# Kernel optimization log

Measured on AMD Instinct MI355X. Metric: run time of the kernel, lower is better.

Reference implementation:

```python
import jax, jax.numpy as jnp
import numpy as np

T, B, OBS, H, ACT = 256, 1024, 256, 256, 64
SLOPE = 0.1


def setup_inputs() -> dict:
    key = jax.random.key(0)
    ks = jax.random.split(key, 20)
    stdv = 1.0 / np.sqrt(H)
    u = lambda k, shape: jax.random.uniform(k, shape, jnp.float32, -stdv, stdv)
    return {
        "x": jax.random.normal(ks[0], (T, B, OBS), jnp.float32),
        "noise1": jax.random.uniform(ks[1], (T, B, 1), jnp.float32),
        "noise2": jax.random.uniform(ks[2], (T, B, 1), jnp.float32),
        # FCEncoder: two Linear+ReLU layers
        "We1": u(ks[3], (OBS, H)), "be1": u(ks[4], (H,)),
        "We2": u(ks[5], (H, H)), "be2": u(ks[6], (H,)),
        # cell_1 (bottom): U_11 [bottom,4H+1], U_21 [top,4H+1], W_01 [H,4H+1], bias
        "U11_1": u(ks[7], (H, 4 * H + 1)), "U21_1": u(ks[8], (H, 4 * H + 1)),
        "W01_1": u(ks[9], (H, 4 * H + 1)), "b1": u(ks[10], (4 * H + 1,)),
        # cell_2 (top, last layer): no U_21
        "U11_2": u(ks[11], (H, 4 * H + 1)), "W01_2": u(ks[12], (H, 4 * H + 1)),
        "b2": u(ks[13], (4 * H + 1,)),
        "Wh": u(ks[14], (H, H)), "bh": u(ks[15], (H,)),
        "Wp": u(ks[16], (H, ACT)), "bp": u(ks[17], (ACT,)),
    }


def _trigger_train(z_hat, noise):
    # forward: (noise < z_hat).float(); backward: 0.1 * identity (straight-through)
    hard = (noise < z_hat).astype(z_hat.dtype)
    return jax.lax.stop_gradient(hard) + 0.1 * (z_hat - jax.lax.stop_gradient(z_hat))


def _gates(f_s):
    f = jax.nn.sigmoid(f_s[:, 0:H])
    i = jax.nn.sigmoid(f_s[:, H:2 * H])
    o = jax.nn.sigmoid(f_s[:, 2 * H:3 * H])
    g = jnp.tanh(f_s[:, 3 * H:4 * H])
    z_hat = jnp.clip((SLOPE * f_s[:, 4 * H:4 * H + 1] + 1.0) / 2.0, 0.05, 0.95)
    return f, i, o, g, z_hat


def reference(x, noise1, noise2, We1, be1, We2, be2,
              U11_1, U21_1, W01_1, b1, U11_2, W01_2, b2, Wh, bh, Wp, bp):
    # encoder over all timesteps at once (parallel_wrapper equivalent)
    xe = jax.nn.relu(jnp.einsum('tbi,ih->tbh', x, We1) + be1)
    xe = jax.nn.relu(jnp.einsum('tbi,ih->tbh', xe, We2) + be2)

    def step(carry, inp):
        h1, c1, z1, h2, c2 = carry
        xt, n1, n2 = inp
        # ---- cell 1 (not last layer; z_bottom = 1) ----
        fs1 = h1 @ W01_1 + z1 * (h2 @ U21_1) + xt @ U11_1 + b1
        f, i, o, g, zhat1 = _gates(fs1)
        c1n = f * c1 + i * g              # z_bottom == 1 everywhere
        h1n = o * jnp.tanh(c1n)
        z1n = _trigger_train(zhat1, n1)
        # ---- cell 2 (last layer; z_bottom = z1n, s_topdown = 0) ----
        fs2 = h2 @ W01_2 + z1n * (h1n @ U11_2) + b2
        f2, i2, o2, g2, zhat2 = _gates(fs2)
        c2n = (1.0 - z1n) * c2 + z1n * (f2 * c2 + i2 * g2)
        h2n = o2 * jnp.tanh(c2n)
        _ = _trigger_train(zhat2, n2)
        return (h1n, c1n, z1n, h2n, c2n), h2n

    zeros = jnp.zeros((B, H), jnp.float32)
    init = (zeros, zeros, jnp.ones((B, 1), jnp.float32), zeros, zeros)
    _, emb = jax.lax.scan(step, init, (xe, noise1, noise2))  # emb: [T,B,H]

    hid = jax.nn.relu(jnp.einsum('tbh,hk->tbk', emb, Wh) + bh)
    pred = jnp.tanh(jnp.einsum('tbh,ha->tba', hid, Wp) + bp)
    return pred
```

## Files before the change

### kernel.cpp

```cpp
#include <hip/hip_runtime.h>
#include <math.h>

typedef __attribute__((ext_vector_type(8))) _Float16 half8;
typedef __attribute__((ext_vector_type(4))) float    f32x4;
typedef unsigned long long u64;

#define NSTEP 256
#define CH    32
#define NCHUNK (NSTEP/CH)
#define NB    1024
#define HID   256
#define BH    262144
#define LK    40
#define LK1   776
#define LW2   520
#define INV2K 4.8828125e-4f

#define W1H_OFF 0
#define W1L_OFF 49664
#define W2H_OFF 99328
#define WZ_OFF  132608
#define PAN_OFF 135680
#define SEQ_SMEM 135936

__device__ __forceinline__ float sigf(float x){ return 1.f/(1.f+expf(-x)); }
__device__ __forceinline__ void splitf(float v, _Float16& h, _Float16& l){
    h = (_Float16)v; l = (_Float16)((v - (float)h)*2048.f);
}

__global__ __launch_bounds__(256)
void wsplit_k(const float* __restrict__ s0, const float* __restrict__ s1,
              const float* __restrict__ s2, int K, int N, int ldn,
              int kb1, int kb2, int perm,
              _Float16* __restrict__ oh, _Float16* __restrict__ ol)
{
    int idx = blockIdx.x*256 + threadIdx.x;
    if (idx >= N*K) return;
    int n = idx / K, k = idx - n*K;
    int jsrc = perm ? ((n&3)*256 + (n>>2)) : n;
    const float* s = (k < kb1) ? &s0[(size_t)k*ldn]
                   : (k < kb2) ? &s1[(size_t)(k-kb1)*ldn]
                               : &s2[(size_t)(k-kb2)*ldn];
    float v = s[jsrc];
    _Float16 h, l; splitf(v, h, l);
    oh[idx] = h; ol[idx] = l;
}

__global__ void wz_k(const float* __restrict__ W01, const float* __restrict__ U21,
                     const float* __restrict__ U11, float* __restrict__ wz)
{
    int k = blockIdx.x*256 + threadIdx.x;
    if (k >= 768) return;
    wz[k] = (k < 256) ? W01[(size_t)k*1025 + 1024]
          : (k < 512) ? U21[(size_t)(k-256)*1025 + 1024]
                      : U11[(size_t)(k-512)*1025 + 1024];
}

__global__ __launch_bounds__(256)
void init_k(_Float16* h1H, _Float16* h1L, _Float16* h2H, _Float16* h2L,
            float* c1g, float* c2g, unsigned* zcb)
{
    int i = blockIdx.x*256 + threadIdx.x;
    h1H[i] = (_Float16)0.f; h1L[i] = (_Float16)0.f;
    h2H[i] = (_Float16)0.f; h2L[i] = (_Float16)0.f;
    c1g[i] = 0.f; c2g[i] = 0.f;
    if (i < NB) zcb[i] = 1u;
}

template<int AIN, int AOUT, int NCOL>
__global__ __launch_bounds__(256)
void gemm_t(const float* __restrict__ Af,
            const _Float16* __restrict__ Ah_, const _Float16* __restrict__ Al_,
            const _Float16* __restrict__ Bh_, const _Float16* __restrict__ Bl_,
            const float* __restrict__ bias,
            _Float16* __restrict__ Oh, _Float16* __restrict__ Ol,
            float* __restrict__ Of)
{
    constexpr int NT = 8;
    __shared__ __align__(16) char smem[40960];

    const int tid  = threadIdx.x;
    const size_t R0 = (size_t)blockIdx.x*64;
    const int C0   = blockIdx.y*64;
    const int rh   = (tid>>6)&1, ch = tid>>7;
    const int lane = tid&63, lr = lane&15, kq = (lane>>4)<<3;
    const int arow = tid>>2, seg = tid&3;
    const size_t abase = (R0+arow)*256 + seg*8;
    const size_t wbase = (size_t)(C0 + (tid>>2))*256 + seg*8;

    f32x4 am[2][2], ax[2][2];
#pragma unroll
    for (int r=0;r<2;++r)
#pragma unroll
        for (int c=0;c<2;++c){ am[r][c]=(f32x4)0.f; ax[r][c]=(f32x4)0.f; }

    half8 rah, ral, rwh, rwl;
    auto load_tile = [&](int k0, half8& ah, half8& al, half8& wh, half8& wl) {
        if (AIN == 0) {
            float4 a0 = *(const float4*)(Af + abase + k0);
            float4 a1 = *(const float4*)(Af + abase + k0 + 4);
            float av[8] = {a0.x,a0.y,a0.z,a0.w,a1.x,a1.y,a1.z,a1.w};
#pragma unroll
            for (int i=0;i<8;++i){ _Float16 h,l; splitf(av[i],h,l); ah[i]=h; al[i]=l; }
        } else {
            ah = *(const half8*)(Ah_ + abase + k0);
            al = *(const half8*)(Al_ + abase + k0);
        }
        wh = *(const half8*)(Bh_ + wbase + k0);
        wl = *(const half8*)(Bl_ + wbase + k0);
    };
    auto store_tile = [&](int buf) {
        char* bs = smem + buf*20480;
        *(half8*)((_Float16*)(bs        ) + arow*LK + seg*8) = rah;
        *(half8*)((_Float16*)(bs +  5120) + arow*LK + seg*8) = ral;
        *(half8*)((_Float16*)(bs + 10240) + (tid>>2)*LK + seg*8) = rwh;
        *(half8*)((_Float16*)(bs + 15360) + (tid>>2)*LK + seg*8) = rwl;
    };

    load_tile(0, rah, ral, rwh, rwl);
    store_tile(0);

#pragma unroll 2
    for (int kb = 0; kb < NT; ++kb) {
        const int buf = kb & 1;
        half8 nah, nal, nwh, nwl;
        if (kb+1 < NT) load_tile((kb+1)*32, nah, nal, nwh, nwl);
        __syncthreads();
        const char* bs = smem + buf*20480;
        const _Float16* LAh = (const _Float16*)bs;
        const _Float16* LAl = (const _Float16*)(bs +  5120);
        const _Float16* LBh = (const _Float16*)(bs + 10240);
        const _Float16* LBl = (const _Float16*)(bs + 15360);
        half8 fah[2], fal[2], fbh[2], fbl[2];
#pragma unroll
        for (int rf=0;rf<2;++rf) {
            fah[rf] = *(const half8*)(LAh + (rh*32+rf*16+lr)*LK + kq);
            fal[rf] = *(const half8*)(LAl + (rh*32+rf*16+lr)*LK + kq);
        }
#pragma unroll
        for (int cf=0;cf<2;++cf) {
            fbh[cf] = *(const half8*)(LBh + (ch*32+cf*16+lr)*LK + kq);
            fbl[cf] = *(const half8*)(LBl + (ch*32+cf*16+lr)*LK + kq);
        }
#pragma unroll
        for (int cf=0;cf<2;++cf)
#pragma unroll
            for (int rf=0;rf<2;++rf) {
                am[rf][cf] = __builtin_amdgcn_mfma_f32_16x16x32_f16(fah[rf], fbh[cf], am[rf][cf],0,0,0);
                ax[rf][cf] = __builtin_amdgcn_mfma_f32_16x16x32_f16(fah[rf], fbl[cf], ax[rf][cf],0,0,0);
                ax[rf][cf] = __builtin_amdgcn_mfma_f32_16x16x32_f16(fal[rf], fbh[cf], ax[rf][cf],0,0,0);
            }
        if (kb+1 < NT) {
            rah=nah; ral=nal; rwh=nwh; rwl=nwl;
            store_tile((kb+1)&1);
        }
    }

#pragma unroll
    for (int cf=0;cf<2;++cf) {
        int col = C0 + ch*32 + cf*16 + lr;
        float bcol = bias[col];
#pragma unroll
        for (int rf=0;rf<2;++rf)
#pragma unroll
            for (int q=0;q<4;++q) {
                size_t row = R0 + rh*32 + rf*16 + ((lane>>4)<<2) + q;
                float v = am[rf][cf][q] + ax[rf][cf][q]*INV2K + bcol;
                if (AOUT == 0) {
                    v = fmaxf(v, 0.f);
                    _Float16 h,l; splitf(v,h,l);
                    Oh[row*NCOL + col] = h;
                    Ol[row*NCOL + col] = l;
                } else {
                    Of[row*NCOL + col] = tanhf(v);
                }
            }
    }
}

struct PArgs {
    const _Float16 *XeH, *XeL;
    _Float16 *EmH, *EmL;
    const _Float16 *W1h, *W1l, *W2h, *W2l;
    const float *b1, *b2, *wz, *noise;
    _Float16 *h1rH, *h1rL, *h2rH, *h2rL;
    unsigned *zcb;
    float *c1g, *c2g;
    unsigned *ctr;
    unsigned *tick;
    int chunk;
};

__device__ __forceinline__ void barrier_arrive(unsigned* c, int tid)
{
    __syncthreads();
    if (tid == 0)
        __hip_atomic_fetch_add(c, 1u, __ATOMIC_RELAXED, __HIP_MEMORY_SCOPE_AGENT);
}
__device__ __forceinline__ void barrier_wait(unsigned* c, int tid)
{
    if (tid == 0) {
        int guard = 0;
        while (__hip_atomic_load(c, __ATOMIC_RELAXED, __HIP_MEMORY_SCOPE_AGENT) < 32u
               && guard < (1<<16)) {
            __builtin_amdgcn_s_sleep(2);
            ++guard;
        }
    }
    __syncthreads();
}

__global__ __launch_bounds__(512, 1)
void hm_pers_k(PArgs a)
{
    extern __shared__ __align__(16) char smem[];

    const int tid = threadIdx.x, wv = tid>>6, lane = tid&63;
    const int lr = lane&15, hq = lane>>4, kg8 = hq<<3;

    unsigned* pan_sh = (unsigned*)(smem + PAN_OFF);
    if (tid == 0) {
        unsigned xcc;
        asm volatile("s_getreg_b32 %0, hwreg(HW_REG_XCC_ID)" : "=s"(xcc));
        xcc &= 7u;
        unsigned slot = __hip_atomic_fetch_add(a.tick + a.chunk*8 + xcc, 1u,
                          __ATOMIC_RELAXED, __HIP_MEMORY_SCOPE_AGENT);
        pan_sh[0] = xcc;
        pan_sh[1] = slot & 31u;
    }
    __syncthreads();
    const int panel = pan_sh[0], cs = pan_sh[1];
    const int R0 = panel*128, hb = cs*8;
    const int row = R0 + wv*16 + lr;
    const size_t rbase = (size_t)row*HID;
    const int hc0 = hb + hq, hc1 = hb + 4 + hq;

    float b1v[2][4], b2v[2][4];
#pragma unroll
    for (int cf=0; cf<2; ++cf)
#pragma unroll
        for (int q=0;q<4;++q) {
            int hc = hb + cf*4 + hq;
            b1v[cf][q] = a.b1[q*256 + hc];
            b2v[cf][q] = a.b2[q*256 + hc];
        }
    const float b1z = a.b1[1024];

#pragma unroll
    for (int it = 0; it < 12; ++it) {
        int idx = it*512 + tid;
        int hl  = idx >= 3072;
        int e   = idx - hl*3072;
        int c   = e / 96;
        int ks  = e - c*96;
        const _Float16* src = (hl ? a.W1l : a.W1h)
            + (size_t)(cs*32 + c)*768 + ks*8;
        *(half8*)(smem + (hl ? W1L_OFF : W1H_OFF) + (c*LK1 + ks*8)*2)
            = *(const half8*)src;
    }
#pragma unroll
    for (int it = 0; it < 4; ++it) {
        int idx = it*512 + tid;
        int c   = idx >> 6;
        int ks  = idx & 63;
        const _Float16* src = a.W2h + (size_t)(cs*32 + c)*512 + ks*8;
        *(half8*)(smem + W2H_OFF + (c*LW2 + ks*8)*2) = *(const half8*)src;
    }
    {
        float* wzl = (float*)(smem + WZ_OFF);
        for (int i = tid; i < 768; i += 512) wzl[i] = a.wz[i];
    }
    __syncthreads();
    const float* wzl = (const float*)(smem + WZ_OFF);

    float c1s[2] = { a.c1g[rbase + hc0], a.c1g[rbase + hc1] };
    float c2s[2] = { a.c2g[rbase + hc0], a.c2g[rbase + hc1] };
    bool zrv = a.zcb[row] != 0u;

    const _Float16* w2lp[2] = {
        a.W2l + (size_t)(cs*32      + lr)*512 + kg8,
        a.W2l + (size_t)(cs*32 + 16 + lr)*512 + kg8
    };

    half8 pf_h[4], pf_l[4];
#pragma unroll
    for (int kt = 0; kt < 4; ++kt) {
        pf_h[kt] = *(const half8*)(a.h1rH + rbase + kt*32 + kg8);
        pf_l[kt] = *(const half8*)(a.h1rL + rbase + kt*32 + kg8);
    }

#pragma unroll 1
    for (int s = 0; s < CH; ++s) {
        const int t = a.chunk*CH + s;
        const _Float16* h1cH = a.h1rH + (size_t)s*BH;
        const _Float16* h1cL = a.h1rL + (size_t)s*BH;
        _Float16*       h1nH = a.h1rH + (size_t)(s+1)*BH;
        _Float16*       h1nL = a.h1rL + (size_t)(s+1)*BH;
        const _Float16* h2cH = a.h2rH + (size_t)s*BH;
        const _Float16* h2cL = a.h2rL + (size_t)s*BH;
        _Float16*       h2nH = a.h2rH + (size_t)(s+1)*BH;
        _Float16*       h2nL = a.h2rL + (size_t)(s+1)*BH;
        const _Float16* xeh = a.XeH + (size_t)t*BH;
        const _Float16* xel = a.XeL + (size_t)t*BH;

        auto ld1 = [&](int kt, half8& h, half8& l){
            const int k0 = kt*32;
            if (k0 < 256)      { h = *(const half8*)(h1cH + rbase + k0 + kg8);
                                 l = *(const half8*)(h1cL + rbase + k0 + kg8); }
            else if (k0 < 512) { h = *(const half8*)(h2cH + rbase + (k0-256) + kg8);
                                 l = *(const half8*)(h2cL + rbase + (k0-256) + kg8); }
            else               { h = *(const half8*)(xeh + rbase + (k0-512) + kg8);
                                 l = *(const half8*)(xel + rbase + (k0-512) + kg8); }
        };
        auto ld2 = [&](int kt, half8& h, half8& l){
            const int k0 = kt*32;
            if (k0 < 256) { h = *(const half8*)(h2cH + rbase + k0 + kg8);
                            l = *(const half8*)(h2cL + rbase + k0 + kg8); }
            else          { h = *(const half8*)(h1nH + rbase + (k0-256) + kg8);
                            l = *(const half8*)(h1nL + rbase + (k0-256) + kg8); }
        };

        f32x4 am[2], ax[2];
        am[0]=(f32x4)0.f; am[1]=(f32x4)0.f; ax[0]=(f32x4)0.f; ax[1]=(f32x4)0.f;
        float zacc = 0.f;

#pragma unroll
        for (int kt = 0; kt < 24; ++kt) {
            half8 sh = pf_h[kt&3], sl = pf_l[kt&3];
            if (kt+4 < 24) ld1(kt+4, pf_h[kt&3], pf_l[kt&3]);
            if (kt >= 8 && kt < 16 && !zrv) { sh = half8{}; sl = half8{}; }
#pragma unroll
            for (int i = 0; i < 8; ++i)
                zacc = fmaf((float)sh[i] + (float)sl[i]*INV2K,
                            wzl[kt*32 + kg8 + i], zacc);
#pragma unroll
            for (int cf = 0; cf < 2; ++cf) {
                const int wb = (cf*16 + lr)*LK1 + kt*32 + kg8;
                half8 wh = *(const half8*)((const _Float16*)(smem + W1H_OFF) + wb);
                half8 wl = *(const half8*)((const _Float16*)(smem + W1L_OFF) + wb);
                am[cf] = __builtin_amdgcn_mfma_f32_16x16x32_f16(wh, sh, am[cf],0,0,0);
                ax[cf] = __builtin_amdgcn_mfma_f32_16x16x32_f16(wl, sh, ax[cf],0,0,0);
                ax[cf] = __builtin_amdgcn_mfma_f32_16x16x32_f16(wh, sl, ax[cf],0,0,0);
            }
        }
        zacc += __shfl_xor(zacc, 16);
        zacc += __shfl_xor(zacc, 32);

        float fsz = zacc + b1z;
        float zh = fminf(fmaxf((0.1f*fsz + 1.f)*0.5f, 0.05f), 0.95f);
        const bool znv = a.noise[(size_t)t*NB + row] < zh;

#pragma unroll
        for (int cf = 0; cf < 2; ++cf) {
            float v0 = am[cf][0] + ax[cf][0]*INV2K + b1v[cf][0];
            float v1 = am[cf][1] + ax[cf][1]*INV2K + b1v[cf][1];
            float v2 = am[cf][2] + ax[cf][2]*INV2K + b1v[cf][2];
            float v3 = am[cf][3] + ax[cf][3]*INV2K + b1v[cf][3];
            float f = sigf(v0), i = sigf(v1), o = sigf(v2), g = tanhf(v3);
            float cn = f*c1s[cf] + i*g;
            c1s[cf] = cn;
            float hn = o*tanhf(cn);
            _Float16 hh, hl; splitf(hn, hh, hl);
            const int hc = (cf==0) ? hc0 : hc1;
            h1nH[rbase + hc] = hh; h1nL[rbase + hc] = hl;
            if (s == CH-1) { a.h1rH[rbase + hc] = hh; a.h1rL[rbase + hc] = hl; }
        }
        if (s == CH-1 && hq == 0) a.zcb[row] = znv ? 1u : 0u;

        unsigned* b1c = a.ctr + ((size_t)(a.chunk*CH + s)*2 + 0)*8 + panel;
        barrier_arrive(b1c, tid);

        am[0]=(f32x4)0.f; am[1]=(f32x4)0.f; ax[0]=(f32x4)0.f; ax[1]=(f32x4)0.f;
#pragma unroll
        for (int kt = 0; kt < 4; ++kt) ld2(kt, pf_h[kt], pf_l[kt]);
#pragma unroll
        for (int kt = 0; kt < 8; ++kt) {
            half8 sh = pf_h[kt&3], sl = pf_l[kt&3];
            if (kt+4 < 8) ld2(kt+4, pf_h[kt&3], pf_l[kt&3]);
#pragma unroll
            for (int cf = 0; cf < 2; ++cf) {
                const int wb = (cf*16 + lr)*LW2 + kt*32 + kg8;
                half8 wh = *(const half8*)((const _Float16*)(smem + W2H_OFF) + wb);
                half8 wl = *(const half8*)(w2lp[cf] + kt*32);
                am[cf] = __builtin_amdgcn_mfma_f32_16x16x32_f16(wh, sh, am[cf],0,0,0);
                ax[cf] = __builtin_amdgcn_mfma_f32_16x16x32_f16(wl, sh, ax[cf],0,0,0);
                ax[cf] = __builtin_amdgcn_mfma_f32_16x16x32_f16(wh, sl, ax[cf],0,0,0);
            }
        }
        barrier_wait(b1c, tid);

#pragma unroll
        for (int kt = 8; kt < 12; ++kt) ld2(kt, pf_h[kt&3], pf_l[kt&3]);
#pragma unroll
        for (int kt = 8; kt < 16; ++kt) {
            half8 sh = pf_h[kt&3], sl = pf_l[kt&3];
            if (kt+4 < 16) ld2(kt+4, pf_h[kt&3], pf_l[kt&3]);
            if (!znv) { sh = half8{}; sl = half8{}; }
#pragma unroll
            for (int cf = 0; cf < 2; ++cf) {
                const int wb = (cf*16 + lr)*LW2 + kt*32 + kg8;
                half8 wh = *(const half8*)((const _Float16*)(smem + W2H_OFF) + wb);
                half8 wl = *(const half8*)(w2lp[cf] + kt*32);
                am[cf] = __builtin_amdgcn_mfma_f32_16x16x32_f16(wh, sh, am[cf],0,0,0);
                ax[cf] = __builtin_amdgcn_mfma_f32_16x16x32_f16(wl, sh, ax[cf],0,0,0);
                ax[cf] = __builtin_amdgcn_mfma_f32_16x16x32_f16(wh, sl, ax[cf],0,0,0);
            }
        }

#pragma unroll
        for (int cf = 0; cf < 2; ++cf) {
            float v0 = am[cf][0] + ax[cf][0]*INV2K + b2v[cf][0];
            float v1 = am[cf][1] + ax[cf][1]*INV2K + b2v[cf][1];
            float v2 = am[cf][2] + ax[cf][2]*INV2K + b2v[cf][2];
            float v3 = am[cf][3] + ax[cf][3]*INV2K + b2v[cf][3];
            float f = sigf(v0), i = sigf(v1), o = sigf(v2), g = tanhf(v3);
            float cn = znv ? (f*c2s[cf] + i*g) : c2s[cf];
            c2s[cf] = cn;
            float hn = o*tanhf(cn);
            _Float16 hh, hl; splitf(hn, hh, hl);
            const int hc = (cf==0) ? hc0 : hc1;
            h2nH[rbase + hc] = hh; h2nL[rbase + hc] = hl;
            a.EmH[(size_t)t*BH + rbase + hc] = hh;
            a.EmL[(size_t)t*BH + rbase + hc] = hl;
            if (s == CH-1) { a.h2rH[rbase + hc] = hh; a.h2rL[rbase + hc] = hl; }
        }
        zrv = znv;

        unsigned* b2c = a.ctr + ((size_t)(a.chunk*CH + s)*2 + 1)*8 + panel;
        barrier_arrive(b2c, tid);
        if (s+1 < CH) {
#pragma unroll
            for (int kt = 0; kt < 4; ++kt) {
                pf_h[kt] = *(const half8*)(h1nH + rbase + kt*32 + kg8);
                pf_l[kt] = *(const half8*)(h1nL + rbase + kt*32 + kg8);
            }
        }
        barrier_wait(b2c, tid);
    }

    a.c1g[rbase + hc0] = c1s[0]; a.c1g[rbase + hc1] = c1s[1];
    a.c2g[rbase + hc0] = c2s[0]; a.c2g[rbase + hc1] = c2s[1];
}

extern "C" void kernel_launch(void* const* d_in, const int* in_sizes, int n_in,
                              void* d_out, int out_size, void* d_ws, size_t ws_size,
                              hipStream_t stream)
{
    const float* x     = (const float*)d_in[0];
    const float* n1    = (const float*)d_in[1];
    const float* We1   = (const float*)d_in[3];
    const float* be1   = (const float*)d_in[4];
    const float* We2   = (const float*)d_in[5];
    const float* be2   = (const float*)d_in[6];
    const float* U11_1 = (const float*)d_in[7];
    const float* U21_1 = (const float*)d_in[8];
    const float* W01_1 = (const float*)d_in[9];
    const float* b1    = (const float*)d_in[10];
    const float* U11_2 = (const float*)d_in[11];
    const float* W01_2 = (const float*)d_in[12];
    const float* b2    = (const float*)d_in[13];
    const float* Wh    = (const float*)d_in[14];
    const float* bh    = (const float*)d_in[15];
    const float* Wp    = (const float*)d_in[16];
    const float* bp_   = (const float*)d_in[17];
    float* out = (float*)d_out;

    char* p = (char*)d_ws;
    auto alloc = [&](size_t bytes){ char* q = p; p += (bytes + 255) & ~(size_t)255; return q; };
    _Float16* XeH  = (_Float16*)alloc((size_t)NSTEP*BH*2);
    _Float16* XeL  = (_Float16*)alloc((size_t)NSTEP*BH*2);
    _Float16* EmH  = (_Float16*)alloc((size_t)NSTEP*BH*2);
    _Float16* EmL  = (_Float16*)alloc((size_t)NSTEP*BH*2);
    _Float16* Wt1h = (_Float16*)alloc((size_t)1024*768*2);
    _Float16* Wt1l = (_Float16*)alloc((size_t)1024*768*2);
    _Float16* Wt2h = (_Float16*)alloc((size_t)1024*512*2);
    _Float16* Wt2l = (_Float16*)alloc((size_t)1024*512*2);
    _Float16* We1h = (_Float16*)alloc(256*256*2);
    _Float16* We1l = (_Float16*)alloc(256*256*2);
    _Float16* We2h = (_Float16*)alloc(256*256*2);
    _Float16* We2l = (_Float16*)alloc(256*256*2);
    _Float16* Whh  = (_Float16*)alloc(256*256*2);
    _Float16* Whl  = (_Float16*)alloc(256*256*2);
    _Float16* Wph  = (_Float16*)alloc(64*256*2);
    _Float16* Wpl  = (_Float16*)alloc(64*256*2);
    float*    wz1  = (float*)alloc(768*4);
    _Float16* h1rH = (_Float16*)alloc((size_t)(CH+1)*BH*2);
    _Float16* h1rL = (_Float16*)alloc((size_t)(CH+1)*BH*2);
    _Float16* h2rH = (_Float16*)alloc((size_t)(CH+1)*BH*2);
    _Float16* h2rL = (_Float16*)alloc((size_t)(CH+1)*BH*2);
    unsigned* zcb  = (unsigned*)alloc(NB*4);
    float*    c1g  = (float*)alloc((size_t)BH*4);
    float*    c2g  = (float*)alloc((size_t)BH*4);
    unsigned* ctr  = (unsigned*)alloc((size_t)NCHUNK*CH*2*8*4);
    unsigned* tick = (unsigned*)alloc((size_t)NCHUNK*8*4);
    if (ws_size < (size_t)(p - (char*)d_ws)) return;

    _Float16* TmpH = EmH; _Float16* TmpL = EmL;
    _Float16* TpH  = XeH; _Float16* TpL  = XeL;

    wsplit_k<<<dim3(3072), 256, 0, stream>>>(W01_1, U21_1, U11_1, 768, 1024, 1025, 256, 512, 1, Wt1h, Wt1l);
    wsplit_k<<<dim3(2048), 256, 0, stream>>>(W01_2, U11_2, nullptr, 512, 1024, 1025, 256, 512, 1, Wt2h, Wt2l);
    wsplit_k<<<dim3(256),  256, 0, stream>>>(We1, nullptr, nullptr, 256, 256, 256, 256, 256, 0, We1h, We1l);
    wsplit_k<<<dim3(256),  256, 0, stream>>>(We2, nullptr, nullptr, 256, 256, 256, 256, 256, 0, We2h, We2l);
    wsplit_k<<<dim3(256),  256, 0, stream>>>(Wh,  nullptr, nullptr, 256, 256, 256, 256, 256, 0, Whh,  Whl);
    wsplit_k<<<dim3(64),   256, 0, stream>>>(Wp,  nullptr, nullptr, 256, 64, 64, 256, 256, 0, Wph, Wpl);
    wz_k<<<dim3(3), 256, 0, stream>>>(W01_1, U21_1, U11_1, wz1);
    init_k<<<dim3(1024), 256, 0, stream>>>(h1rH, h1rL, h2rH, h2rL, c1g, c2g, zcb);
    (void)hipMemsetAsync(ctr, 0, (size_t)NCHUNK*CH*2*8*4, stream);
    (void)hipMemsetAsync(tick, 0, (size_t)NCHUNK*8*4, stream);

    for (int c = 0; c < 8; ++c) {
        size_t ro = (size_t)c*32*BH;
        gemm_t<0,0,256><<<dim3(512,4), 256, 0, stream>>>(
            x + ro, nullptr, nullptr, We1h, We1l, be1, TmpH, TmpL, nullptr);
        gemm_t<1,0,256><<<dim3(512,4), 256, 0, stream>>>(
            nullptr, TmpH, TmpL, We2h, We2l, be2, XeH + ro, XeL + ro, nullptr);
    }

    (void)hipFuncSetAttribute((const void*)hm_pers_k,
        hipFuncAttributeMaxDynamicSharedMemorySize, SEQ_SMEM);
    PArgs pa;
    pa.XeH = XeH; pa.XeL = XeL; pa.EmH = EmH; pa.EmL = EmL;
    pa.W1h = Wt1h; pa.W1l = Wt1l; pa.W2h = Wt2h; pa.W2l = Wt2l;
    pa.b1 = b1; pa.b2 = b2; pa.wz = wz1; pa.noise = n1;
    pa.h1rH = h1rH; pa.h1rL = h1rL; pa.h2rH = h2rH; pa.h2rL = h2rL;
    pa.zcb = zcb; pa.c1g = c1g; pa.c2g = c2g; pa.ctr = ctr; pa.tick = tick;
    for (int c = 0; c < NCHUNK; ++c) {
        pa.chunk = c;
        void* kargs[] = { (void*)&pa };
        (void)hipLaunchCooperativeKernel((const void*)hm_pers_k, dim3(256), dim3(512),
                                         kargs, SEQ_SMEM, stream);
    }

    for (int c = 0; c < 8; ++c) {
        size_t ro = (size_t)c*32*BH;
        gemm_t<1,0,256><<<dim3(512,4), 256, 0, stream>>>(
            nullptr, EmH + ro, EmL + ro, Whh, Whl, bh, TpH, TpL, nullptr);
        gemm_t<1,1,64><<<dim3(512,1), 256, 0, stream>>>(
            nullptr, TpH, TpL, Wph, Wpl, bp_, nullptr, nullptr,
            out + (size_t)c*32*NB*64);
    }
}
```

Measured before the change: 8.243 ms.

## Split persistent recurrence across 512 blocks with smaller per-block weight slices

```diff
diff --git a/kernel.cpp b/kernel.cpp
--- a/kernel.cpp
+++ b/kernel.cpp
@@ -11,17 +11,15 @@
 #define NB    1024
 #define HID   256
 #define BH    262144
+#define NPAN  16
 #define LK    40
-#define LK1   776
+#define LK1H  712
 #define LW2   520
 #define INV2K 4.8828125e-4f
 
 #define W1H_OFF 0
-#define W1L_OFF 49664
-#define W2H_OFF 99328
-#define WZ_OFF  132608
-#define PAN_OFF 135680
-#define SEQ_SMEM 135936
+#define W2H_OFF 45568
+#define SEQ_SMEM 79872
 
 __device__ __forceinline__ float sigf(float x){ return 1.f/(1.f+expf(-x)); }
 __device__ __forceinline__ void splitf(float v, _Float16& h, _Float16& l){
@@ -202,61 +200,59 @@
     if (tid == 0) {
         int guard = 0;
         while (__hip_atomic_load(c, __ATOMIC_RELAXED, __HIP_MEMORY_SCOPE_AGENT) < 32u
-               && guard < (1<<16)) {
-            __builtin_amdgcn_s_sleep(2);
+               && guard < (1<<17)) {
+            __builtin_amdgcn_s_sleep(1);
             ++guard;
         }
     }
     __syncthreads();
 }
 
-__global__ __launch_bounds__(512, 1)
+__global__ __launch_bounds__(512, 4)
 void hm_pers_k(PArgs a)
 {
     extern __shared__ __align__(16) char smem[];
 
     const int tid = threadIdx.x, wv = tid>>6, lane = tid&63;
     const int lr = lane&15, hq = lane>>4, kg8 = hq<<3;
-
-    unsigned* pan_sh = (unsigned*)(smem + PAN_OFF);
+    const int rg = wv & 3, cg = wv >> 2;
+
+    unsigned* pan_sh = (unsigned*)smem;
     if (tid == 0) {
         unsigned xcc;
         asm volatile("s_getreg_b32 %0, hwreg(HW_REG_XCC_ID)" : "=s"(xcc));
         xcc &= 7u;
         unsigned slot = __hip_atomic_fetch_add(a.tick + a.chunk*8 + xcc, 1u,
                           __ATOMIC_RELAXED, __HIP_MEMORY_SCOPE_AGENT);
-        pan_sh[0] = xcc;
-        pan_sh[1] = slot & 31u;
+        pan_sh[0] = xcc*2u + (slot & 1u);
+        pan_sh[1] = (slot >> 1) & 31u;
     }
     __syncthreads();
     const int panel = pan_sh[0], cs = pan_sh[1];
-    const int R0 = panel*128, hb = cs*8;
-    const int row = R0 + wv*16 + lr;
+    __syncthreads();
+
+    const int R0 = panel*64, hb = cs*8;
+    const int row = R0 + rg*16 + lr;
     const size_t rbase = (size_t)row*HID;
-    const int hc0 = hb + hq, hc1 = hb + 4 + hq;
-
-    float b1v[2][4], b2v[2][4];
-#pragma unroll
-    for (int cf=0; cf<2; ++cf)
-#pragma unroll
-        for (int q=0;q<4;++q) {
-            int hc = hb + cf*4 + hq;
-            b1v[cf][q] = a.b1[q*256 + hc];
-            b2v[cf][q] = a.b2[q*256 + hc];
-        }
+    const int hc = hb + cg*4 + hq;
+
+    float b1v[4], b2v[4];
+#pragma unroll
+    for (int q=0;q<4;++q) {
+        b1v[q] = a.b1[q*256 + hc];
+        b2v[q] = a.b2[q*256 + hc];
+    }
     const float b1z = a.b1[1024];
 
 #pragma unroll
-    for (int it = 0; it < 12; ++it) {
+    for (int it = 0; it < 6; ++it) {
         int idx = it*512 + tid;
-        int hl  = idx >= 3072;
-        int e   = idx - hl*3072;
-        int c   = e / 96;
-        int ks  = e - c*96;
-        const _Float16* src = (hl ? a.W1l : a.W1h)
-            + (size_t)(cs*32 + c)*768 + ks*8;
-        *(half8*)(smem + (hl ? W1L_OFF : W1H_OFF) + (c*LK1 + ks*8)*2)
-            = *(const half8*)src;
+        if (idx < 2816) {
+            int c  = idx / 88;
+            int ks = idx - c*88;
+            const _Float16* src = a.W1h + (size_t)(cs*32 + c)*768 + ks*8;
+            *(half8*)(smem + W1H_OFF + (c*LK1H + ks*8)*2) = *(const half8*)src;
+        }
     }
 #pragma unroll
     for (int it = 0; it < 4; ++it) {
@@ -266,21 +262,17 @@
         const _Float16* src = a.W2h + (size_t)(cs*32 + c)*512 + ks*8;
         *(half8*)(smem + W2H_OFF + (c*LW2 + ks*8)*2) = *(const half8*)src;
     }
-    {
-        float* wzl = (float*)(smem + WZ_OFF);
-        for (int i = tid; i < 768; i += 512) wzl[i] = a.wz[i];
-    }
     __syncthreads();
-    const float* wzl = (const float*)(smem + WZ_OFF);
-
-    float c1s[2] = { a.c1g[rbase + hc0], a.c1g[rbase + hc1] };
-    float c2s[2] = { a.c2g[rbase + hc0], a.c2g[rbase + hc1] };
+
+    float c1s = a.c1g[rbase + hc];
+    float c2s = a.c2g[rbase + hc];
     bool zrv = a.zcb[row] != 0u;
 
-    const _Float16* w2lp[2] = {
-        a.W2l + (size_t)(cs*32      + lr)*512 + kg8,
-        a.W2l + (size_t)(cs*32 + 16 + lr)*512 + kg8
-    };
+    const int wcol = cs*32 + cg*16 + lr;
+    const int lcol = cg*16 + lr;
+    const _Float16* W1hp = a.W1h + (size_t)wcol*768 + kg8;
+    const _Float16* W1lp = a.W1l + (size_t)wcol*768 + kg8;
+    const _Float16* W2lp = a.W2l + (size_t)wcol*512 + kg8;
 
     half8 pf_h[4], pf_l[4];
 #pragma unroll
@@ -320,8 +312,7 @@
                             l = *(const half8*)(h1nL + rbase + (k0-256) + kg8); }
         };
 
-        f32x4 am[2], ax[2];
-        am[0]=(f32x4)0.f; am[1]=(f32x4)0.f; ax[0]=(f32x4)0.f; ax[1]=(f32x4)0.f;
+        f32x4 am = (f32x4)0.f, ax = (f32x4)0.f;
         float zacc = 0.f;
 
 #pragma unroll
@@ -332,16 +323,17 @@
 #pragma unroll
             for (int i = 0; i < 8; ++i)
                 zacc = fmaf((float)sh[i] + (float)sl[i]*INV2K,
-                            wzl[kt*32 + kg8 + i], zacc);
-#pragma unroll
-            for (int cf = 0; cf < 2; ++cf) {
-                const int wb = (cf*16 + lr)*LK1 + kt*32 + kg8;
-                half8 wh = *(const half8*)((const _Float16*)(smem + W1H_OFF) + wb);
-                half8 wl = *(const half8*)((const _Float16*)(smem + W1L_OFF) + wb);
-                am[cf] = __builtin_amdgcn_mfma_f32_16x16x32_f16(wh, sh, am[cf],0,0,0);
-                ax[cf] = __builtin_amdgcn_mfma_f32_16x16x32_f16(wl, sh, ax[cf],0,0,0);
-                ax[cf] = __builtin_amdgcn_mfma_f32_16x16x32_f16(wh, sl, ax[cf],0,0,0);
-            }
+                            a.wz[kt*32 + kg8 + i], zacc);
+            half8 wh;
+            if (kt < 22)
+                wh = *(const half8*)((const _Float16*)(smem + W1H_OFF)
+                                     + lcol*LK1H + kt*32 + kg8);
+            else
+                wh = *(const half8*)(W1hp + kt*32);
+            half8 wl = *(const half8*)(W1lp + kt*32);
+            am = __builtin_amdgcn_mfma_f32_16x16x32_f16(wh, sh, am,0,0,0);
+            ax = __builtin_amdgcn_mfma_f32_16x16x32_f16(wl, sh, ax,0,0,0);
+            ax = __builtin_amdgcn_mfma_f32_16x16x32_f16(wh, sl, ax,0,0,0);
         }
         zacc += __shfl_xor(zacc, 16);
         zacc += __shfl_xor(zacc, 32);
@@ -350,42 +342,37 @@
         float zh = fminf(fmaxf((0.1f*fsz + 1.f)*0.5f, 0.05f), 0.95f);
         const bool znv = a.noise[(size_t)t*NB + row] < zh;
 
-#pragma unroll
-        for (int cf = 0; cf < 2; ++cf) {
-            float v0 = am[cf][0] + ax[cf][0]*INV2K + b1v[cf][0];
-            float v1 = am[cf][1] + ax[cf][1]*INV2K + b1v[cf][1];
-            float v2 = am[cf][2] + ax[cf][2]*INV2K + b1v[cf][2];
-            float v3 = am[cf][3] + ax[cf][3]*INV2K + b1v[cf][3];
+        {
+            float v0 = am[0] + ax[0]*INV2K + b1v[0];
+            float v1 = am[1] + ax[1]*INV2K + b1v[1];
+            float v2 = am[2] + ax[2]*INV2K + b1v[2];
+            float v3 = am[3] + ax[3]*INV2K + b1v[3];
             float f = sigf(v0), i = sigf(v1), o = sigf(v2), g = tanhf(v3);
-            float cn = f*c1s[cf] + i*g;
-            c1s[cf] = cn;
+            float cn = f*c1s + i*g;
+            c1s = cn;
             float hn = o*tanhf(cn);
             _Float16 hh, hl; splitf(hn, hh, hl);
-            const int hc = (cf==0) ? hc0 : hc1;
             h1nH[rbase + hc] = hh; h1nL[rbase + hc] = hl;
             if (s == CH-1) { a.h1rH[rbase + hc] = hh; a.h1rL[rbase + hc] = hl; }
         }
-        if (s == CH-1 && hq == 0) a.zcb[row] = znv ? 1u : 0u;
-
-        unsigned* b1c = a.ctr + ((size_t)(a.chunk*CH + s)*2 + 0)*8 + panel;
+        if (s == CH-1 && cg == 0 && hq == 0) a.zcb[row] = znv ? 1u : 0u;
+
+        unsigned* b1c = a.ctr + ((size_t)(a.chunk*CH + s)*2 + 0)*NPAN + panel;
         barrier_arrive(b1c, tid);
 
-        am[0]=(f32x4)0.f; am[1]=(f32x4)0.f; ax[0]=(f32x4)0.f; ax[1]=(f32x4)0.f;
+        am = (f32x4)0.f; ax = (f32x4)0.f;
 #pragma unroll
         for (int kt = 0; kt < 4; ++kt) ld2(kt, pf_h[kt], pf_l[kt]);
 #pragma unroll
         for (int kt = 0; kt < 8; ++kt) {
             half8 sh = pf_h[kt&3], sl = pf_l[kt&3];
             if (kt+4 < 8) ld2(kt+4, pf_h[kt&3], pf_l[kt&3]);
-#pragma unroll
-            for (int cf = 0; cf < 2; ++cf) {
-                const int wb = (cf*16 + lr)*LW2 + kt*32 + kg8;
-                half8 wh = *(const half8*)((const _Float16*)(smem + W2H_OFF) + wb);
-                half8 wl = *(const half8*)(w2lp[cf] + kt*32);
-                am[cf] = __builtin_amdgcn_mfma_f32_16x16x32_f16(wh, sh, am[cf],0,0,0);
-                ax[cf] = __builtin_amdgcn_mfma_f32_16x16x32_f16(wl, sh, ax[cf],0,0,0);
-                ax[cf] = __builtin_amdgcn_mfma_f32_16x16x32_f16(wh, sl, ax[cf],0,0,0);
-            }
+            half8 wh = *(const half8*)((const _Float16*)(smem + W2H_OFF)
+                                       + lcol*LW2 + kt*32 + kg8);
+            half8 wl = *(const half8*)(W2lp + kt*32);
+            am = __builtin_amdgcn_mfma_f32_16x16x32_f16(wh, sh, am,0,0,0);
+            ax = __builtin_amdgcn_mfma_f32_16x16x32_f16(wl, sh, ax,0,0,0);
+            ax = __builtin_amdgcn_mfma_f32_16x16x32_f16(wh, sl, ax,0,0,0);
         }
         barrier_wait(b1c, tid);
 
@@ -396,29 +383,24 @@
             half8 sh = pf_h[kt&3], sl = pf_l[kt&3];
             if (kt+4 < 16) ld2(kt+4, pf_h[kt&3], pf_l[kt&3]);
             if (!znv) { sh = half8{}; sl = half8{}; }
-#pragma unroll
-            for (int cf = 0; cf < 2; ++cf) {
-                const int wb = (cf*16 + lr)*LW2 + kt*32 + kg8;
-                half8 wh = *(const half8*)((const _Float16*)(smem + W2H_OFF) + wb);
-                half8 wl = *(const half8*)(w2lp[cf] + kt*32);
-                am[cf] = __builtin_amdgcn_mfma_f32_16x16x32_f16(wh, sh, am[cf],0,0,0);
-                ax[cf] = __builtin_amdgcn_mfma_f32_16x16x32_f16(wl, sh, ax[cf],0,0,0);
-                ax[cf] = __builtin_amdgcn_mfma_f32_16x16x32_f16(wh, sl, ax[cf],0,0,0);
-            }
-        }
-
-#pragma unroll
-        for (int cf = 0; cf < 2; ++cf) {
-            float v0 = am[cf][0] + ax[cf][0]*INV2K + b2v[cf][0];
-            float v1 = am[cf][1] + ax[cf][1]*INV2K + b2v[cf][1];
-            float v2 = am[cf][2] + ax[cf][2]*INV2K + b2v[cf][2];
-            float v3 = am[cf][3] + ax[cf][3]*INV2K + b2v[cf][3];
+            half8 wh = *(const half8*)((const _Float16*)(smem + W2H_OFF)
+                                       + lcol*LW2 + kt*32 + kg8);
+            half8 wl = *(const half8*)(W2lp + kt*32);
+            am = __builtin_amdgcn_mfma_f32_16x16x32_f16(wh, sh, am,0,0,0);
+            ax = __builtin_amdgcn_mfma_f32_16x16x32_f16(wl, sh, ax,0,0,0);
+            ax = __builtin_amdgcn_mfma_f32_16x16x32_f16(wh, sl, ax,0,0,0);
+        }
+
+        {
+            float v0 = am[0] + ax[0]*INV2K + b2v[0];
+            float v1 = am[1] + ax[1]*INV2K + b2v[1];
+            float v2 = am[2] + ax[2]*INV2K + b2v[2];
+            float v3 = am[3] + ax[3]*INV2K + b2v[3];
             float f = sigf(v0), i = sigf(v1), o = sigf(v2), g = tanhf(v3);
-            float cn = znv ? (f*c2s[cf] + i*g) : c2s[cf];
-            c2s[cf] = cn;
+            float cn = znv ? (f*c2s + i*g) : c2s;
+            c2s = cn;
             float hn = o*tanhf(cn);
             _Float16 hh, hl; splitf(hn, hh, hl);
-            const int hc = (cf==0) ? hc0 : hc1;
             h2nH[rbase + hc] = hh; h2nL[rbase + hc] = hl;
             a.EmH[(size_t)t*BH + rbase + hc] = hh;
             a.EmL[(size_t)t*BH + rbase + hc] = hl;
@@ -426,7 +408,7 @@
         }
         zrv = znv;
 
-        unsigned* b2c = a.ctr + ((size_t)(a.chunk*CH + s)*2 + 1)*8 + panel;
+        unsigned* b2c = a.ctr + ((size_t)(a.chunk*CH + s)*2 + 1)*NPAN + panel;
         barrier_arrive(b2c, tid);
         if (s+1 < CH) {
 #pragma unroll
@@ -438,8 +420,8 @@
         barrier_wait(b2c, tid);
     }
 
-    a.c1g[rbase + hc0] = c1s[0]; a.c1g[rbase + hc1] = c1s[1];
-    a.c2g[rbase + hc0] = c2s[0]; a.c2g[rbase + hc1] = c2s[1];
+    a.c1g[rbase + hc] = c1s;
+    a.c2g[rbase + hc] = c2s;
 }
 
 extern "C" void kernel_launch(void* const* d_in, const int* in_sizes, int n_in,
@@ -491,7 +473,7 @@
     unsigned* zcb  = (unsigned*)alloc(NB*4);
     float*    c1g  = (float*)alloc((size_t)BH*4);
     float*    c2g  = (float*)alloc((size_t)BH*4);
-    unsigned* ctr  = (unsigned*)alloc((size_t)NCHUNK*CH*2*8*4);
+    unsigned* ctr  = (unsigned*)alloc((size_t)NCHUNK*CH*2*NPAN*4);
     unsigned* tick = (unsigned*)alloc((size_t)NCHUNK*8*4);
     if (ws_size < (size_t)(p - (char*)d_ws)) return;
 
@@ -506,7 +488,7 @@
     wsplit_k<<<dim3(64),   256, 0, stream>>>(Wp,  nullptr, nullptr, 256, 64, 64, 256, 256, 0, Wph, Wpl);
     wz_k<<<dim3(3), 256, 0, stream>>>(W01_1, U21_1, U11_1, wz1);
     init_k<<<dim3(1024), 256, 0, stream>>>(h1rH, h1rL, h2rH, h2rL, c1g, c2g, zcb);
-    (void)hipMemsetAsync(ctr, 0, (size_t)NCHUNK*CH*2*8*4, stream);
+    (void)hipMemsetAsync(ctr, 0, (size_t)NCHUNK*CH*2*NPAN*4, stream);
     (void)hipMemsetAsync(tick, 0, (size_t)NCHUNK*8*4, stream);
 
     for (int c = 0; c < 8; ++c) {
@@ -527,9 +509,7 @@
     pa.zcb = zcb; pa.c1g = c1g; pa.c2g = c2g; pa.ctr = ctr; pa.tick = tick;
     for (int c = 0; c < NCHUNK; ++c) {
         pa.chunk = c;
-        void* kargs[] = { (void*)&pa };
-        (void)hipLaunchCooperativeKernel((const void*)hm_pers_k, dim3(256), dim3(512),
-                                         kargs, SEQ_SMEM, stream);
+        hm_pers_k<<<dim3(512), dim3(512), SEQ_SMEM, stream>>>(pa);
     }
 
     for (int c = 0; c < 8; ++c) {
```

Measured after the change: 21.07 ms. 156% more time.
